# Kernel optimization log

Measured on AMD Instinct MI355X. Metric: run time of the kernel, lower is better.

Reference implementation:

```python
import jax, jax.numpy as jnp
import numpy as np

B, T, D, H, O = 256, 512, 128, 128, 64


def setup_inputs() -> dict:
    key = jax.random.key(0)
    ks = jax.random.split(key, 10)
    s = 1.0 / np.sqrt(H)
    u = lambda k, shape: jax.random.uniform(k, shape, jnp.float32, -s, s)
    return {
        "x": jax.random.normal(ks[0], (B, T, D), jnp.float32),
        "W_ih": u(ks[1], (4 * H, D)),   # torch gate order: i, f, g, o
        "W_hh": u(ks[2], (4 * H, H)),
        "b_ih": u(ks[3], (4 * H,)),
        "b_hh": u(ks[4], (4 * H,)),
        "W1": u(ks[5], (H, H)),
        "b1": u(ks[6], (H,)),
        "W2": u(ks[7], (O, H)),
        "b2": u(ks[8], (O,)),
    }


def lstm_scan(x, W_ih, W_hh, b_ih, b_hh):
    b, t, _ = x.shape
    h4 = W_hh.shape[0] // 4
    # precompute input contribution for all timesteps (one big GEMM)
    xg = jnp.einsum('btd,gd->btg', x, W_ih) + b_ih + b_hh  # (B,T,4H)
    xg = jnp.swapaxes(xg, 0, 1)  # (T,B,4H) for scan over time

    def step(carry, xg_t):
        h, c = carry
        g = xg_t + h @ W_hh.T  # (B,4H)
        i, f, gg, o = jnp.split(g, 4, axis=-1)
        i = jax.nn.sigmoid(i)
        f = jax.nn.sigmoid(f)
        gg = jnp.tanh(gg)
        o = jax.nn.sigmoid(o)
        c = f * c + i * gg
        h = o * jnp.tanh(c)
        return (h, c), h

    h0 = jnp.zeros((b, h4), x.dtype)
    c0 = jnp.zeros((b, h4), x.dtype)
    _, hs = jax.lax.scan(step, (h0, c0), xg)  # hs: (T,B,H)
    return jnp.swapaxes(hs, 0, 1)  # (B,T,H), matching torch batch_first


def reference(x, W_ih, W_hh, b_ih, b_hh, W1, b1, W2, b2):
    b, t, _ = x.shape
    h = lstm_scan(x, W_ih, W_hh, b_ih, b_hh)          # (B,T,H)
    hflat = h.reshape(-1, h.shape[-1])                 # (B*T,H), b-major (as torch)
    hflat = hflat @ W1.T + b1
    y = hflat @ W2.T + b2                              # (B*T,O)
    # faithful to original: reshape flattened b-major rows as (T,B,O), take [-1]
    y = y.reshape(t, b, -1)
    return y[-1]                                       # (B,O)
```

## Files before the change

kernel.cpp:

```cpp
#include <hip/hip_runtime.h>
#include <math.h>

#define BB 256
#define TT 512
#define DD 128
#define HH 128
#define GG 512
#define OO 64
#define NCH (TT / 4)

typedef _Float16 half8 __attribute__((ext_vector_type(8)));
typedef float    f32x4 __attribute__((ext_vector_type(4)));

__device__ __forceinline__ float sigmoid_fast(float x) {
    return 1.0f / (1.0f + __expf(-x));
}
__device__ __forceinline__ float tanh_fast(float x) {
    float ax = fabsf(x);
    float e = __expf(2.0f * ax);
    float t = 1.0f - 2.0f / (e + 1.0f);
    return copysignf(t, x);
}

__global__ __launch_bounds__(512) void xgpack_kernel(
    const float* __restrict__ x,
    const float* __restrict__ W_ih,
    const float* __restrict__ b_ih,
    const float* __restrict__ b_hh,
    const float* __restrict__ W_hh,
    float* __restrict__ xg,
    _Float16* __restrict__ Wp)
{
    if (blockIdx.x >= TT) {
        const int g = (blockIdx.x - TT) * 512 + threadIdx.x;
        const int fid = g >> 6, l = g & 63;
        const int w = fid >> 5, rem = fid & 31, nt = rem >> 2, kt = rem & 3;
        const int quad = l >> 4, col = l & 15;
        const int row = (nt >> 1) * 128 + (nt & 1) * 16 + w * 32 + col;
        const int off = kt * 32 + quad * 8;
        const float* s = W_hh + row * HH + off;
        _Float16* d = Wp + (size_t)g * 8;
#pragma unroll
        for (int i = 0; i < 8; i++) d[i] = (_Float16)s[i];
        return;
    }

    const int t = blockIdx.x;
    const int g = threadIdx.x;

    __shared__ __align__(16) float xs[DD];
    if (g < DD) xs[g] = x[(255 * TT + t) * DD + g];
    __syncthreads();

    const float4* __restrict__ wrow = (const float4*)(W_ih + g * DD);
    const float4* __restrict__ xv   = (const float4*)xs;

    float a0 = 0.f, a1 = 0.f, a2 = 0.f, a3 = 0.f;
#pragma unroll
    for (int i = 0; i < DD / 4; i += 4) {
        float4 w0 = wrow[i + 0], w1 = wrow[i + 1], w2 = wrow[i + 2], w3 = wrow[i + 3];
        float4 h0 = xv[i + 0],  h1 = xv[i + 1],  h2 = xv[i + 2],  h3 = xv[i + 3];
        a0 += w0.x * h0.x + w0.y * h0.y + w0.z * h0.z + w0.w * h0.w;
        a1 += w1.x * h1.x + w1.y * h1.y + w1.z * h1.z + w1.w * h1.w;
        a2 += w2.x * h2.x + w2.y * h2.y + w2.z * h2.z + w2.w * h2.w;
        a3 += w3.x * h3.x + w3.y * h3.y + w3.z * h3.z + w3.w * h3.w;
    }
    const float val = (a0 + a1) + (a2 + a3) + b_ih[g] + b_hh[g];
    xg[t * GG + (g & 127) * 4 + (g >> 7)] = val;
}

__global__
__attribute__((amdgpu_flat_work_group_size(256, 256), amdgpu_waves_per_eu(1, 1)))
void scan_kernel(
    const _Float16* __restrict__ Wp,
    const float* __restrict__ xgp,
    float* __restrict__ hs)
{
    const int tid  = threadIdx.x;
    const int lane = tid & 63;
    const int w    = tid >> 6;
    const int col  = lane & 15;
    const int quad = lane >> 4;
    const int wbase = w * 32;
    const bool sel  = (lane >= 32);
    const int jsel  = wbase + (sel ? 16 : 0) + col;
    const int aoff  = quad * 8;

    __shared__ __align__(16) _Float16 h_lds[2][HH];
    __shared__ __align__(16) float xgc[2][4][HH][4];
    __shared__ __align__(16) float hs_l[BB * HH];

#define BLOADP(nt, kt) \
    half8 B##nt##_##kt = *(const half8*)(Wp + (((w * 32 + (nt) * 4 + (kt)) * 64 + lane) * 8));
#define FOR_KT(X, nt) X(nt, 0) X(nt, 1) X(nt, 2) X(nt, 3)
#define FOR_NT(X) FOR_KT(X, 0) FOR_KT(X, 1) FOR_KT(X, 2) FOR_KT(X, 3) \
                  FOR_KT(X, 4) FOR_KT(X, 5) FOR_KT(X, 6) FOR_KT(X, 7)
    FOR_NT(BLOADP)

    asm volatile("" : "+v"(B0_0), "+v"(B0_1), "+v"(B0_2), "+v"(B0_3),
                      "+v"(B1_0), "+v"(B1_1), "+v"(B1_2), "+v"(B1_3),
                      "+v"(B2_0), "+v"(B2_1), "+v"(B2_2), "+v"(B2_3),
                      "+v"(B3_0), "+v"(B3_1), "+v"(B3_2), "+v"(B3_3));
    asm volatile("" : "+v"(B4_0), "+v"(B4_1), "+v"(B4_2), "+v"(B4_3),
                      "+v"(B5_0), "+v"(B5_1), "+v"(B5_2), "+v"(B5_3),
                      "+v"(B6_0), "+v"(B6_1), "+v"(B6_2), "+v"(B6_3),
                      "+v"(B7_0), "+v"(B7_1), "+v"(B7_2), "+v"(B7_3));

    if (tid < HH) h_lds[0][tid] = (_Float16)0.f;

    {
        const f32x4* src = (const f32x4*)xgp;
        f32x4 a = src[2 * tid], b = src[2 * tid + 1];
        f32x4* dst = (f32x4*)&xgc[0][0][0][0];
        dst[2 * tid] = a; dst[2 * tid + 1] = b;
    }
    float c = 0.f;
    int p = 0;
    __syncthreads();

    f32x4 pf0, pf1;

    for (int ch = 0; ch < NCH; ch++) {
        const int buf = ch & 1;
        if (ch + 1 < NCH) {
            const f32x4* src = (const f32x4*)(xgp + (ch + 1) * 4 * GG);
            pf0 = src[2 * tid];
            pf1 = src[2 * tid + 1];
        }
#pragma unroll
        for (int k = 0; k < 4; k++) {
            const int t = ch * 4 + k;

            const _Float16* hl = h_lds[p];
            half8 A0 = *(const half8*)(hl + 0 * 32 + aoff);
            half8 A1 = *(const half8*)(hl + 1 * 32 + aoff);
            half8 A2 = *(const half8*)(hl + 2 * 32 + aoff);
            half8 A3 = *(const half8*)(hl + 3 * 32 + aoff);

            f32x4 xgv = *(const f32x4*)&xgc[buf][k][jsel][0];

            f32x4 C0 = {0.f,0.f,0.f,0.f}, C1 = {0.f,0.f,0.f,0.f};
            f32x4 C2 = {0.f,0.f,0.f,0.f}, C3 = {0.f,0.f,0.f,0.f};
            f32x4 C4 = {0.f,0.f,0.f,0.f}, C5 = {0.f,0.f,0.f,0.f};
            f32x4 C6 = {0.f,0.f,0.f,0.f}, C7 = {0.f,0.f,0.f,0.f};
#define MF(nt, kt) \
            C##nt = __builtin_amdgcn_mfma_f32_16x16x32_f16(A##kt, B##nt##_##kt, C##nt, 0, 0, 0);
#define MF_ALLNT(kt) MF(0, kt) MF(1, kt) MF(2, kt) MF(3, kt) \
                     MF(4, kt) MF(5, kt) MF(6, kt) MF(7, kt)
            MF_ALLNT(0) MF_ALLNT(1) MF_ALLNT(2) MF_ALLNT(3)
#undef MF_ALLNT
#undef MF

            float pi = (sel ? C1[0] : C0[0]) + xgv.x;
            float pf = (sel ? C3[0] : C2[0]) + xgv.y;
            float pg = (sel ? C5[0] : C4[0]) + xgv.z;
            float po = (sel ? C7[0] : C6[0]) + xgv.w;

            float iv = sigmoid_fast(pi);
            float fv = sigmoid_fast(pf);
            float gv = tanh_fast(pg);
            float ov = sigmoid_fast(po);

            c = fv * c + iv * gv;
            float hval = ov * tanh_fast(c);

            if (quad == 0 || quad == 3) {
                h_lds[1 - p][jsel] = (_Float16)hval;
                if (t >= TT - BB) hs_l[(t - (TT - BB)) * HH + jsel] = hval;
            }

            if (k == 3 && ch + 1 < NCH) {
                f32x4* dst = (f32x4*)&xgc[1 - buf][0][0][0];
                dst[2 * tid] = pf0;
                dst[2 * tid + 1] = pf1;
            }

            p ^= 1;
            __syncthreads();
        }
    }

    const f32x4* s = (const f32x4*)hs_l;
    f32x4* d = (f32x4*)hs;
#pragma unroll 4
    for (int i = tid; i < BB * HH / 4; i += 256) d[i] = s[i];
}

__global__ __launch_bounds__(128) void mlp_kernel(
    const float* __restrict__ hs,
    const float* __restrict__ W1,
    const float* __restrict__ b1,
    const float* __restrict__ W2,
    const float* __restrict__ b2,
    float* __restrict__ out)
{
    const int r = blockIdx.x;
    const int j = threadIdx.x;

    __shared__ __align__(16) float hsh[HH];
    __shared__ __align__(16) float z[HH];

    hsh[j] = hs[r * HH + j];
    __syncthreads();

    {
        const float4* __restrict__ wrow = (const float4*)(W1 + j * HH);
        const float4* __restrict__ hv   = (const float4*)hsh;
        float acc = b1[j];
#pragma unroll
        for (int i = 0; i < 32; i++) {
            float4 ww = wrow[i], h = hv[i];
            acc += ww.x * h.x + ww.y * h.y + ww.z * h.z + ww.w * h.w;
        }
        z[j] = acc;
    }
    __syncthreads();

    if (j < OO) {
        const float4* __restrict__ wrow = (const float4*)(W2 + j * HH);
        const float4* __restrict__ zv   = (const float4*)z;
        float acc = b2[j];
#pragma unroll
        for (int i = 0; i < 32; i++) {
            float4 ww = wrow[i], zz = zv[i];
            acc += ww.x * zz.x + ww.y * zz.y + ww.z * zz.z + ww.w * zz.w;
        }
        out[r * OO + j] = acc;
    }
}

extern "C" void kernel_launch(void* const* d_in, const int* in_sizes, int n_in,
                              void* d_out, int out_size, void* d_ws, size_t ws_size,
                              hipStream_t stream) {
    const float* x    = (const float*)d_in[0];
    const float* W_ih = (const float*)d_in[1];
    const float* W_hh = (const float*)d_in[2];
    const float* b_ih = (const float*)d_in[3];
    const float* b_hh = (const float*)d_in[4];
    const float* W1   = (const float*)d_in[5];
    const float* b1   = (const float*)d_in[6];
    const float* W2   = (const float*)d_in[7];
    const float* b2   = (const float*)d_in[8];
    float* out = (float*)d_out;

    float*    xg = (float*)d_ws;
    float*    hs = xg + TT * GG;
    _Float16* Wp = (_Float16*)(hs + BB * HH);

    xgpack_kernel<<<TT + 16, 512, 0, stream>>>(x, W_ih, b_ih, b_hh, W_hh, xg, Wp);
    scan_kernel<<<1, 256, 0, stream>>>(Wp, xg, hs);
    mlp_kernel<<<BB, 128, 0, stream>>>(hs, W1, b1, W2, b2, out);
}
```

Before: 384.9 us.

## Prefetch xg into registers and stream hidden states straight to global in scan

```diff
diff --git a/kernel.cpp b/kernel.cpp
--- a/kernel.cpp
+++ b/kernel.cpp
@@ -7,18 +7,16 @@
 #define HH 128
 #define GG 512
 #define OO 64
-#define NCH (TT / 4)
 
 typedef _Float16 half8 __attribute__((ext_vector_type(8)));
 typedef float    f32x4 __attribute__((ext_vector_type(4)));
 
 __device__ __forceinline__ float sigmoid_fast(float x) {
-    return 1.0f / (1.0f + __expf(-x));
+    return __builtin_amdgcn_rcpf(1.0f + __expf(-x));
 }
 __device__ __forceinline__ float tanh_fast(float x) {
-    float ax = fabsf(x);
-    float e = __expf(2.0f * ax);
-    float t = 1.0f - 2.0f / (e + 1.0f);
+    float e = __expf(2.0f * fabsf(x));
+    float t = fmaf(-2.0f, __builtin_amdgcn_rcpf(e + 1.0f), 1.0f);
     return copysignf(t, x);
 }
 
@@ -85,10 +83,9 @@
     const bool sel  = (lane >= 32);
     const int jsel  = wbase + (sel ? 16 : 0) + col;
     const int aoff  = quad * 8;
+    const bool wr   = (quad == 0) || (quad == 3);
 
     __shared__ __align__(16) _Float16 h_lds[2][HH];
-    __shared__ __align__(16) float xgc[2][4][HH][4];
-    __shared__ __align__(16) float hs_l[BB * HH];
 
 #define BLOADP(nt, kt) \
     half8 B##nt##_##kt = *(const half8*)(Wp + (((w * 32 + (nt) * 4 + (kt)) * 64 + lane) * 8));
@@ -108,82 +105,62 @@
 
     if (tid < HH) h_lds[0][tid] = (_Float16)0.f;
 
-    {
-        const f32x4* src = (const f32x4*)xgp;
-        f32x4 a = src[2 * tid], b = src[2 * tid + 1];
-        f32x4* dst = (f32x4*)&xgc[0][0][0][0];
-        dst[2 * tid] = a; dst[2 * tid + 1] = b;
-    }
+    f32x4 Z = {0.f, 0.f, 0.f, 0.f};
+    asm volatile("" : "+v"(Z));
+
+    const float* __restrict__ xgl = xgp + jsel * 4;
+    f32x4 xg0 = *(const f32x4*)(xgl + 0 * GG);
+    f32x4 xg1 = *(const f32x4*)(xgl + 1 * GG);
+
     float c = 0.f;
-    int p = 0;
-    __syncthreads();
-
-    f32x4 pf0, pf1;
-
-    for (int ch = 0; ch < NCH; ch++) {
-        const int buf = ch & 1;
-        if (ch + 1 < NCH) {
-            const f32x4* src = (const f32x4*)(xgp + (ch + 1) * 4 * GG);
-            pf0 = src[2 * tid];
-            pf1 = src[2 * tid + 1];
-        }
-#pragma unroll
-        for (int k = 0; k < 4; k++) {
-            const int t = ch * 4 + k;
-
-            const _Float16* hl = h_lds[p];
-            half8 A0 = *(const half8*)(hl + 0 * 32 + aoff);
-            half8 A1 = *(const half8*)(hl + 1 * 32 + aoff);
-            half8 A2 = *(const half8*)(hl + 2 * 32 + aoff);
-            half8 A3 = *(const half8*)(hl + 3 * 32 + aoff);
-
-            f32x4 xgv = *(const f32x4*)&xgc[buf][k][jsel][0];
-
-            f32x4 C0 = {0.f,0.f,0.f,0.f}, C1 = {0.f,0.f,0.f,0.f};
-            f32x4 C2 = {0.f,0.f,0.f,0.f}, C3 = {0.f,0.f,0.f,0.f};
-            f32x4 C4 = {0.f,0.f,0.f,0.f}, C5 = {0.f,0.f,0.f,0.f};
-            f32x4 C6 = {0.f,0.f,0.f,0.f}, C7 = {0.f,0.f,0.f,0.f};
-#define MF(nt, kt) \
-            C##nt = __builtin_amdgcn_mfma_f32_16x16x32_f16(A##kt, B##nt##_##kt, C##nt, 0, 0, 0);
-#define MF_ALLNT(kt) MF(0, kt) MF(1, kt) MF(2, kt) MF(3, kt) \
-                     MF(4, kt) MF(5, kt) MF(6, kt) MF(7, kt)
-            MF_ALLNT(0) MF_ALLNT(1) MF_ALLNT(2) MF_ALLNT(3)
-#undef MF_ALLNT
-#undef MF
-
-            float pi = (sel ? C1[0] : C0[0]) + xgv.x;
-            float pf = (sel ? C3[0] : C2[0]) + xgv.y;
-            float pg = (sel ? C5[0] : C4[0]) + xgv.z;
-            float po = (sel ? C7[0] : C6[0]) + xgv.w;
-
-            float iv = sigmoid_fast(pi);
-            float fv = sigmoid_fast(pf);
-            float gv = tanh_fast(pg);
-            float ov = sigmoid_fast(po);
-
-            c = fv * c + iv * gv;
-            float hval = ov * tanh_fast(c);
-
-            if (quad == 0 || quad == 3) {
-                h_lds[1 - p][jsel] = (_Float16)hval;
-                if (t >= TT - BB) hs_l[(t - (TT - BB)) * HH + jsel] = hval;
-            }
-
-            if (k == 3 && ch + 1 < NCH) {
-                f32x4* dst = (f32x4*)&xgc[1 - buf][0][0][0];
-                dst[2 * tid] = pf0;
-                dst[2 * tid + 1] = pf1;
-            }
-
-            p ^= 1;
-            __syncthreads();
-        }
-    }
-
-    const f32x4* s = (const f32x4*)hs_l;
-    f32x4* d = (f32x4*)hs;
-#pragma unroll 4
-    for (int i = tid; i < BB * HH / 4; i += 256) d[i] = s[i];
+    __syncthreads();
+
+#define MM(a, b, cc) __builtin_amdgcn_mfma_f32_16x16x32_f16((a), (b), (cc), 0, 0, 0)
+#define STEP(par, XCUR) do {                                                            \
+    const int t = t2 + (par);                                                           \
+    f32x4 xpf = *(const f32x4*)(xgl + ((t + 2) & (TT - 1)) * GG);                       \
+    const _Float16* hl = h_lds[(par)];                                                  \
+    half8 A0 = *(const half8*)(hl +  0 + aoff);                                         \
+    half8 A1 = *(const half8*)(hl + 32 + aoff);                                         \
+    half8 A2 = *(const half8*)(hl + 64 + aoff);                                         \
+    half8 A3 = *(const half8*)(hl + 96 + aoff);                                         \
+    f32x4 C0, C1, C2, C3, C4, C5, C6, C7;                                               \
+    C4 = MM(A0, B4_0, Z);  C5 = MM(A0, B5_0, Z);  C0 = MM(A0, B0_0, Z);                 \
+    C1 = MM(A0, B1_0, Z);  C2 = MM(A0, B2_0, Z);  C3 = MM(A0, B3_0, Z);                 \
+    C6 = MM(A0, B6_0, Z);  C7 = MM(A0, B7_0, Z);                                        \
+    C4 = MM(A1, B4_1, C4); C5 = MM(A1, B5_1, C5); C0 = MM(A1, B0_1, C0);                \
+    C1 = MM(A1, B1_1, C1); C2 = MM(A1, B2_1, C2); C3 = MM(A1, B3_1, C3);                \
+    C6 = MM(A1, B6_1, C6); C7 = MM(A1, B7_1, C7);                                       \
+    C4 = MM(A2, B4_2, C4); C5 = MM(A2, B5_2, C5); C0 = MM(A2, B0_2, C0);                \
+    C1 = MM(A2, B1_2, C1); C2 = MM(A2, B2_2, C2); C3 = MM(A2, B3_2, C3);                \
+    C6 = MM(A2, B6_2, C6); C7 = MM(A2, B7_2, C7);                                       \
+    C4 = MM(A3, B4_3, C4); C5 = MM(A3, B5_3, C5); C0 = MM(A3, B0_3, C0);                \
+    C1 = MM(A3, B1_3, C1); C2 = MM(A3, B2_3, C2); C3 = MM(A3, B3_3, C3);                \
+    C6 = MM(A3, B6_3, C6); C7 = MM(A3, B7_3, C7);                                       \
+    float pg = (sel ? C5[0] : C4[0]) + (XCUR).z;                                        \
+    float pi = (sel ? C1[0] : C0[0]) + (XCUR).x;                                        \
+    float pf = (sel ? C3[0] : C2[0]) + (XCUR).y;                                        \
+    float po = (sel ? C7[0] : C6[0]) + (XCUR).w;                                        \
+    float gv = tanh_fast(pg);                                                           \
+    float iv = sigmoid_fast(pi);                                                        \
+    float fv = sigmoid_fast(pf);                                                        \
+    c = fv * c + iv * gv;                                                               \
+    float ov = sigmoid_fast(po);                                                        \
+    float hval = ov * tanh_fast(c);                                                     \
+    if (wr) {                                                                           \
+        h_lds[1 - (par)][jsel] = (_Float16)hval;                                        \
+        hs[(t & (BB - 1)) * HH + jsel] = hval;       \
+    }                                                                                   \
+    asm volatile("s_waitcnt lgkmcnt(0)\n\ts_barrier" ::: "memory");                     \
+    (XCUR) = xpf;                                                                       \
+} while (0)
+
+    for (int t2 = 0; t2 < TT; t2 += 2) {
+        STEP(0, xg0);
+        STEP(1, xg1);
+    }
+#undef STEP
+#undef MM
 }
 
 __global__ __launch_bounds__(128) void mlp_kernel(
```

After: 347.1 us. 9.8% less time.
